# Optimization experiments

Measured on AMD Instinct MI355X. Metric: run time of the kernel, lower is better.

## Reference

```python
import jax, jax.numpy as jnp
import numpy as np

N = 1_000_000
C_IN = 64
COORD_SHIFT = 1024  # keeps shifted coords non-negative (offsets are small)


def setup_inputs() -> dict:
    key = jax.random.key(0)
    ks = jax.random.split(key, 8)
    feats = jax.random.normal(ks[0], (N, C_IN), dtype=jnp.float32)
    coords = jax.random.randint(ks[1], (N, 4), 0, 2048, dtype=jnp.int32)
    mask = jnp.ones((N,), dtype=bool)
    # Pointwise decoder params per decoder_blocks [(64,32),(32,16),(16,3)], bias=True
    s1, s2, s3 = 1.0 / np.sqrt(C_IN), 1.0 / np.sqrt(32), 1.0 / np.sqrt(16)
    W1 = jax.random.normal(ks[2], (C_IN, 32), dtype=jnp.float32) * s1
    b1 = jnp.zeros((32,), dtype=jnp.float32)
    W2 = jax.random.normal(ks[3], (32, 16), dtype=jnp.float32) * s2
    b2 = jnp.zeros((16,), dtype=jnp.float32)
    W3 = jax.random.normal(ks[4], (16, 3), dtype=jnp.float32) * s3
    b3 = jnp.zeros((3,), dtype=jnp.float32)
    return {"feats": feats, "coords": coords, "mask": mask,
            "W1": W1, "b1": b1, "W2": W2, "b2": b2, "W3": W3, "b3": b3}


def _decode(feats, mask, W1, b1, W2, b2, W3, b3):
    # FeatDecoder reduced to its pointwise (kernel-size-1 equivalent) form.
    h = jax.nn.relu(feats @ W1 + b1)
    h = jax.nn.relu(h @ W2 + b2)
    offsets = h @ W3 + b3  # [N, 3]
    return offsets * mask[:, None].astype(offsets.dtype)


def _revoxelize(offsets, coords):
    # offsets_ = [0 | round(offsets)] added to original coords
    off_i = jnp.round(offsets).astype(jnp.int32)                 # [N,3]
    new_coords = coords.at[:, 1:].add(off_i)                     # [N,4]
    # sphash -> unique -> sphashquery == row-wise unique with inverse map
    shifted = new_coords + COORD_SHIFT                           # non-negative rows
    _, inv = jnp.unique(shifted, axis=0, size=N, fill_value=0,
                        return_inverse=True)                      # inv: [N]
    inv = inv.reshape(-1).astype(jnp.int32)
    # spcount: voxels per cluster
    counts = jax.ops.segment_sum(jnp.ones((N,), jnp.float32), inv, num_segments=N)
    # spvoxelize: per-cluster mean of shifted coords, then .int()
    sums = jax.ops.segment_sum(new_coords.astype(jnp.float32), inv, num_segments=N)
    out_coords = (sums / jnp.maximum(counts, 1.0)[:, None]).astype(jnp.int32)
    return out_coords, inv


def reference(feats, coords, mask, W1, b1, W2, b2, W3, b3):
    offsets = _decode(feats, mask, W1, b1, W2, b2, W3, b3)
    out_coords, inv_map = _revoxelize(offsets, coords)
    return offsets, out_coords, inv_map
```

## Files before the change

### kernel.cpp

```cpp
#include <hip/hip_runtime.h>
#include <hip/hip_bf16.h>
#include <stdint.h>


#define TPB 256
#define NB 139264
#define NCHUNK 544
typedef unsigned long long ull;

__global__ __launch_bounds__(256) void k_mlp(
    const float* __restrict__ feats, const int* __restrict__ coords,
    const unsigned char* __restrict__ mask,
    const float* __restrict__ W1, const float* __restrict__ b1,
    const float* __restrict__ W2, const float* __restrict__ b2,
    const float* __restrict__ W3, const float* __restrict__ b3,
    float* __restrict__ out_off, ull* __restrict__ slots,
    unsigned int* __restrict__ cursor, int n)
{
    int i = blockIdx.x * TPB + threadIdx.x;
    if (i >= n) return;

    const float4* f4 = (const float4*)(feats + (size_t)i * 64);

    float h1[32];
    #pragma unroll
    for (int j = 0; j < 32; ++j) h1[j] = 0.0f;
    #pragma unroll
    for (int kc = 0; kc < 16; ++kc) {
        float4 xv = f4[kc];
        #pragma unroll
        for (int d = 0; d < 4; ++d) {
            float x = (d == 0) ? xv.x : (d == 1) ? xv.y : (d == 2) ? xv.z : xv.w;
            const float* wr = W1 + (kc * 4 + d) * 32;
            #pragma unroll
            for (int j = 0; j < 32; j += 4) {
                float4 w = *(const float4*)(wr + j);
                h1[j + 0] = fmaf(x, w.x, h1[j + 0]);
                h1[j + 1] = fmaf(x, w.y, h1[j + 1]);
                h1[j + 2] = fmaf(x, w.z, h1[j + 2]);
                h1[j + 3] = fmaf(x, w.w, h1[j + 3]);
            }
        }
    }
    #pragma unroll
    for (int j = 0; j < 32; ++j) h1[j] = fmaxf(h1[j] + b1[j], 0.0f);

    float h2[16];
    #pragma unroll
    for (int j = 0; j < 16; ++j) h2[j] = 0.0f;
    #pragma unroll
    for (int k = 0; k < 32; ++k) {
        float x = h1[k];
        const float* wr = W2 + k * 16;
        #pragma unroll
        for (int j = 0; j < 16; j += 4) {
            float4 w = *(const float4*)(wr + j);
            h2[j + 0] = fmaf(x, w.x, h2[j + 0]);
            h2[j + 1] = fmaf(x, w.y, h2[j + 1]);
            h2[j + 2] = fmaf(x, w.z, h2[j + 2]);
            h2[j + 3] = fmaf(x, w.w, h2[j + 3]);
        }
    }
    #pragma unroll
    for (int j = 0; j < 16; ++j) h2[j] = fmaxf(h2[j] + b2[j], 0.0f);

    float o0 = 0.0f, o1 = 0.0f, o2 = 0.0f;
    #pragma unroll
    for (int k = 0; k < 16; ++k) {
        float x = h2[k];
        o0 = fmaf(x, W3[k * 3 + 0], o0);
        o1 = fmaf(x, W3[k * 3 + 1], o1);
        o2 = fmaf(x, W3[k * 3 + 2], o2);
    }
    o0 += b3[0]; o1 += b3[1]; o2 += b3[2];

    float m = mask[i] ? 1.0f : 0.0f;
    o0 *= m; o1 *= m; o2 *= m;
    out_off[(size_t)3 * i + 0] = o0;
    out_off[(size_t)3 * i + 1] = o1;
    out_off[(size_t)3 * i + 2] = o2;

    int4 c = ((const int4*)coords)[i];
    int r1 = (int)rintf(o0), r2 = (int)rintf(o1), r3 = (int)rintf(o2);
    int c1u = c.y + r1, c2u = c.z + r2, c3u = c.w + r3;
    int c1s = min(max(c1u + 1024, 0), 8191);
    int c2s = min(max(c2u + 1024, 0), 8191);
    int c3s = min(max(c3u + 1024, 0), 8191);
    int bin1 = min(max((c1u + 64) >> 5, 0), 67);
    int b = c.x * 68 + bin1;
    ull row39 = ((ull)c1s << 26) | ((ull)c2s << 13) | (ull)c3s;
    ull packed = (row39 << 20) | (ull)(unsigned int)i;
    unsigned int j = atomicAdd(&cursor[b], 1u);
    if (j < 64u) slots[(size_t)b * 64 + j] = packed;
}

template<int W>
__device__ inline ull seg_sort(ull v, int lane)
{
    #pragma unroll
    for (int k = 2; k <= W; k <<= 1) {
        #pragma unroll
        for (int j = k >> 1; j > 0; j >>= 1) {
            ull o = __shfl_xor(v, j, 64);
            bool up = ((lane & (k & (W - 1))) == 0);
            bool lower = ((lane & j) == 0);
            ull mn = (v < o) ? v : o;
            ull mx = (v < o) ? o : v;
            v = (up == lower) ? mn : mx;
        }
    }
    return v;
}

__global__ __launch_bounds__(256) void k_passA(
    ull* __restrict__ slots, const unsigned int* __restrict__ cursor,
    unsigned int* __restrict__ ucnt, float* __restrict__ out_inv)
{
    int lane = threadIdx.x & 63;
    int b = blockIdx.x * 4 + (threadIdx.x >> 6);
    unsigned int cnt = cursor[b];
    if (cnt > 64u) cnt = 64u;
    if (cnt == 0u) { if (lane == 0) ucnt[b] = 0u; return; }
    ull v = (lane < (int)cnt) ? slots[(size_t)b * 64 + lane] : ~0ULL;
    if      (cnt <= 8u)  v = seg_sort<8>(v, lane);
    else if (cnt <= 16u) v = seg_sort<16>(v, lane);
    else if (cnt <= 32u) v = seg_sort<32>(v, lane);
    else                 v = seg_sort<64>(v, lane);

    ull row = v >> 20;
    unsigned int idx = (unsigned int)(v & 0xFFFFFULL);
    ull prev = __shfl_up(row, 1, 64);
    bool head = (lane < (int)cnt) && ((lane == 0) || (row != prev));
    ull hm = __ballot(head);
    ull le = (lane == 63) ? ~0ULL : ((1ULL << (lane + 1)) - 1ULL);
    int lrank = __popcll(hm & le) - 1;
    if (lane == 0) ucnt[b] = (unsigned int)__popcll(hm);
    if (lane < (int)cnt)
        ((unsigned int*)out_inv)[idx] = (unsigned int)(b * 64 + lrank);

    int c3s = (int)(row & 0x1FFFULL);
    int c2s = (int)((row >> 13) & 0x1FFFULL);
    int c1s = (int)(row >> 26);
    ull sum = (lane < (int)cnt)
        ? ((1ULL << 57) | ((ull)c1s << 38) | ((ull)c2s << 19) | (ull)c3s)
        : 0ULL;
    ull P = sum;
    #pragma unroll
    for (int d = 1; d < 64; d <<= 1) {
        ull t = __shfl_up(P, d, 64);
        if (lane >= d) P += t;
    }
    ull gt = hm & ~le;
    int tpos = gt ? (__ffsll((long long)gt) - 2) : ((int)cnt - 1);
    ull Pt = __shfl(P, tpos, 64);
    int hsrc = (lane > 0) ? lane - 1 : 0;
    ull Ph = __shfl(P, hsrc, 64);
    if (lane == 0) Ph = 0ULL;
    if (head) slots[(size_t)b * 64 + lrank] = Pt - Ph;
}

__global__ __launch_bounds__(256) void k_scanA(
    const unsigned int* __restrict__ ucnt, unsigned int* __restrict__ lstart,
    unsigned int* __restrict__ chsum)
{
    __shared__ unsigned int s[256];
    int tid = threadIdx.x;
    int g = blockIdx.x * 256 + tid;
    unsigned int v = ucnt[g];
    s[tid] = v;
    __syncthreads();
    for (int ofs = 1; ofs < 256; ofs <<= 1) {
        unsigned int t = (tid >= ofs) ? s[tid - ofs] : 0u;
        __syncthreads();
        s[tid] += t;
        __syncthreads();
    }
    lstart[g] = s[tid] - v;
    if (tid == 255) chsum[blockIdx.x] = s[255];
}

__global__ __launch_bounds__(1024) void k_scanB(unsigned int* __restrict__ chsum)
{
    __shared__ unsigned int s[1024];
    int tid = threadIdx.x;
    unsigned int v = (tid < NCHUNK) ? chsum[tid] : 0u;
    s[tid] = v;
    __syncthreads();
    for (int ofs = 1; ofs < 1024; ofs <<= 1) {
        unsigned int t = (tid >= ofs) ? s[tid - ofs] : 0u;
        __syncthreads();
        s[tid] += t;
        __syncthreads();
    }
    if (tid < NCHUNK) chsum[tid] = s[tid] - v;
}

__global__ __launch_bounds__(256) void k_fixinv(
    float* __restrict__ out_inv, const unsigned int* __restrict__ lstart,
    const unsigned int* __restrict__ chbase, int n)
{
    int i = blockIdx.x * TPB + threadIdx.x;
    if (i >= n) return;
    unsigned int q = ((const unsigned int*)out_inv)[i];
    unsigned int b = q >> 6, lr = q & 63u;
    if (b >= NB) b = NB - 1;
    out_inv[i] = (float)(chbase[b >> 8] + lstart[b] + lr);
}

__global__ __launch_bounds__(256) void k_fixout(
    const ull* __restrict__ slots, const unsigned int* __restrict__ ucnt,
    const unsigned int* __restrict__ lstart, const unsigned int* __restrict__ chbase,
    float* __restrict__ out_oc)
{
    int lane = threadIdx.x & 63;
    int b = blockIdx.x * 4 + (threadIdx.x >> 6);
    unsigned int uc = ucnt[b];
    if (lane >= (int)uc) return;
    ull run = slots[(size_t)b * 64 + lane];
    unsigned int r = chbase[b >> 8] + lstart[b] + (unsigned int)lane;
    int rc = (int)(run >> 57);
    int s1 = (int)((run >> 38) & 0x7FFFFULL) - 1024 * rc;
    int s2 = (int)((run >> 19) & 0x7FFFFULL) - 1024 * rc;
    int s3 = (int)(run & 0x7FFFFULL) - 1024 * rc;
    float fc = (float)rc;
    float4 o;
    o.x = (float)((unsigned int)b / 68u);
    o.y = truncf((float)s1 / fc);
    o.z = truncf((float)s2 / fc);
    o.w = truncf((float)s3 / fc);
    ((float4*)out_oc)[r] = o;
}

extern "C" void kernel_launch(void* const* d_in, const int* in_sizes, int n_in,
                              void* d_out, int out_size, void* d_ws, size_t ws_size,
                              hipStream_t stream)
{
    const float*         feats  = (const float*)d_in[0];
    const int*           coords = (const int*)d_in[1];
    const unsigned char* mask   = (const unsigned char*)d_in[2];
    const float* W1 = (const float*)d_in[3];
    const float* b1 = (const float*)d_in[4];
    const float* W2 = (const float*)d_in[5];
    const float* b2 = (const float*)d_in[6];
    const float* W3 = (const float*)d_in[7];
    const float* b3 = (const float*)d_in[8];

    int n = in_sizes[1] / 4;

    char* ws = (char*)d_ws;
    ull*          slots  = (ull*)ws;
    unsigned int* cursor = (unsigned int*)(ws + (size_t)NB * 64 * 8);
    unsigned int* ucnt   = cursor + NB;
    unsigned int* lstart = ucnt + NB;
    unsigned int* chsum  = lstart + NB;

    float* out     = (float*)d_out;
    float* out_off = out;
    float* out_oc  = out + (size_t)3 * n;
    float* out_inv = out + (size_t)7 * n;

    hipMemsetAsync(cursor, 0, (size_t)NB * sizeof(unsigned int), stream);
    hipMemsetAsync(out_oc, 0, (size_t)4 * n * sizeof(float), stream);

    int nb256 = (n + TPB - 1) / TPB;

    k_mlp<<<nb256, TPB, 0, stream>>>(feats, coords, mask, W1, b1, W2, b2, W3, b3,
                                     out_off, slots, cursor, n);
    k_passA<<<NB / 4, TPB, 0, stream>>>(slots, cursor, ucnt, out_inv);
    k_scanA<<<NCHUNK, 256, 0, stream>>>(ucnt, lstart, chsum);
    k_scanB<<<1, 1024, 0, stream>>>(chsum);
    k_fixinv<<<nb256, TPB, 0, stream>>>(out_inv, lstart, chsum, n);
    k_fixout<<<NB / 4, TPB, 0, stream>>>(slots, ucnt, lstart, chsum, out_oc);
}
```

Before: 543.0 us.

## Fuse inverse-fixup and output-coord kernels, prefetch features, specialize passA scan width

Merges k_fixinv and k_fixout into one per-point kernel, so each point computes its global cluster index and also writes that cluster's mean coordinates. This removes one launch and the separate bucket-parallel pass. Several points of the same cluster now redundantly write identical data, which adds extra slot reads and scattered stores. It also loads all 16 feature vectors up front behind an asm barrier to raise memory-level parallelism in the MLP, and templates passA so the prefix scan runs only over the active width.

```diff
diff --git a/kernel.cpp b/kernel.cpp
--- a/kernel.cpp
+++ b/kernel.cpp
@@ -7,6 +7,7 @@
 #define NB 139264
 #define NCHUNK 544
 typedef unsigned long long ull;
+typedef float vf4 __attribute__((ext_vector_type(4)));
 
 __global__ __launch_bounds__(256) void k_mlp(
     const float* __restrict__ feats, const int* __restrict__ coords,
@@ -20,14 +21,22 @@
     int i = blockIdx.x * TPB + threadIdx.x;
     if (i >= n) return;
 
-    const float4* f4 = (const float4*)(feats + (size_t)i * 64);
+    const vf4* f4 = (const vf4*)(feats + (size_t)i * 64);
+
+    vf4 r[16];
+    #pragma unroll
+    for (int p = 0; p < 16; ++p) r[p] = f4[p];
+    asm volatile("" : "+v"(r[0]), "+v"(r[1]), "+v"(r[2]), "+v"(r[3]),
+                      "+v"(r[4]), "+v"(r[5]), "+v"(r[6]), "+v"(r[7]),
+                      "+v"(r[8]), "+v"(r[9]), "+v"(r[10]), "+v"(r[11]),
+                      "+v"(r[12]), "+v"(r[13]), "+v"(r[14]), "+v"(r[15]));
 
     float h1[32];
     #pragma unroll
     for (int j = 0; j < 32; ++j) h1[j] = 0.0f;
     #pragma unroll
     for (int kc = 0; kc < 16; ++kc) {
-        float4 xv = f4[kc];
+        vf4 xv = r[kc];
         #pragma unroll
         for (int d = 0; d < 4; ++d) {
             float x = (d == 0) ? xv.x : (d == 1) ? xv.y : (d == 2) ? xv.z : xv.w;
@@ -112,20 +121,13 @@
     return v;
 }
 
-__global__ __launch_bounds__(256) void k_passA(
-    ull* __restrict__ slots, const unsigned int* __restrict__ cursor,
-    unsigned int* __restrict__ ucnt, float* __restrict__ out_inv)
-{
-    int lane = threadIdx.x & 63;
-    int b = blockIdx.x * 4 + (threadIdx.x >> 6);
-    unsigned int cnt = cursor[b];
-    if (cnt > 64u) cnt = 64u;
-    if (cnt == 0u) { if (lane == 0) ucnt[b] = 0u; return; }
+template<int W>
+__device__ inline void passA_body(
+    ull* __restrict__ slots, unsigned int* __restrict__ ucnt,
+    unsigned int* __restrict__ inv_bits, int b, int lane, unsigned int cnt)
+{
     ull v = (lane < (int)cnt) ? slots[(size_t)b * 64 + lane] : ~0ULL;
-    if      (cnt <= 8u)  v = seg_sort<8>(v, lane);
-    else if (cnt <= 16u) v = seg_sort<16>(v, lane);
-    else if (cnt <= 32u) v = seg_sort<32>(v, lane);
-    else                 v = seg_sort<64>(v, lane);
+    v = seg_sort<W>(v, lane);
 
     ull row = v >> 20;
     unsigned int idx = (unsigned int)(v & 0xFFFFFULL);
@@ -136,7 +138,7 @@
     int lrank = __popcll(hm & le) - 1;
     if (lane == 0) ucnt[b] = (unsigned int)__popcll(hm);
     if (lane < (int)cnt)
-        ((unsigned int*)out_inv)[idx] = (unsigned int)(b * 64 + lrank);
+        inv_bits[idx] = (unsigned int)(b * 64 + lrank);
 
     int c3s = (int)(row & 0x1FFFULL);
     int c2s = (int)((row >> 13) & 0x1FFFULL);
@@ -146,7 +148,7 @@
         : 0ULL;
     ull P = sum;
     #pragma unroll
-    for (int d = 1; d < 64; d <<= 1) {
+    for (int d = 1; d < W; d <<= 1) {
         ull t = __shfl_up(P, d, 64);
         if (lane >= d) P += t;
     }
@@ -157,6 +159,22 @@
     ull Ph = __shfl(P, hsrc, 64);
     if (lane == 0) Ph = 0ULL;
     if (head) slots[(size_t)b * 64 + lrank] = Pt - Ph;
+}
+
+__global__ __launch_bounds__(256) void k_passA(
+    ull* __restrict__ slots, const unsigned int* __restrict__ cursor,
+    unsigned int* __restrict__ ucnt, float* __restrict__ out_inv)
+{
+    int lane = threadIdx.x & 63;
+    int b = blockIdx.x * 4 + (threadIdx.x >> 6);
+    unsigned int cnt = cursor[b];
+    if (cnt > 64u) cnt = 64u;
+    if (cnt == 0u) { if (lane == 0) ucnt[b] = 0u; return; }
+    unsigned int* inv_bits = (unsigned int*)out_inv;
+    if      (cnt <= 8u)  passA_body<8> (slots, ucnt, inv_bits, b, lane, cnt);
+    else if (cnt <= 16u) passA_body<16>(slots, ucnt, inv_bits, b, lane, cnt);
+    else if (cnt <= 32u) passA_body<32>(slots, ucnt, inv_bits, b, lane, cnt);
+    else                 passA_body<64>(slots, ucnt, inv_bits, b, lane, cnt);
 }
 
 __global__ __launch_bounds__(256) void k_scanA(
@@ -195,8 +213,9 @@
     if (tid < NCHUNK) chsum[tid] = s[tid] - v;
 }
 
-__global__ __launch_bounds__(256) void k_fixinv(
-    float* __restrict__ out_inv, const unsigned int* __restrict__ lstart,
+__global__ __launch_bounds__(256) void k_final(
+    float* __restrict__ out_inv, float* __restrict__ out_oc,
+    const ull* __restrict__ slots, const unsigned int* __restrict__ lstart,
     const unsigned int* __restrict__ chbase, int n)
 {
     int i = blockIdx.x * TPB + threadIdx.x;
@@ -204,31 +223,22 @@
     unsigned int q = ((const unsigned int*)out_inv)[i];
     unsigned int b = q >> 6, lr = q & 63u;
     if (b >= NB) b = NB - 1;
-    out_inv[i] = (float)(chbase[b >> 8] + lstart[b] + lr);
-}
-
-__global__ __launch_bounds__(256) void k_fixout(
-    const ull* __restrict__ slots, const unsigned int* __restrict__ ucnt,
-    const unsigned int* __restrict__ lstart, const unsigned int* __restrict__ chbase,
-    float* __restrict__ out_oc)
-{
-    int lane = threadIdx.x & 63;
-    int b = blockIdx.x * 4 + (threadIdx.x >> 6);
-    unsigned int uc = ucnt[b];
-    if (lane >= (int)uc) return;
-    ull run = slots[(size_t)b * 64 + lane];
-    unsigned int r = chbase[b >> 8] + lstart[b] + (unsigned int)lane;
-    int rc = (int)(run >> 57);
-    int s1 = (int)((run >> 38) & 0x7FFFFULL) - 1024 * rc;
-    int s2 = (int)((run >> 19) & 0x7FFFFULL) - 1024 * rc;
-    int s3 = (int)(run & 0x7FFFFULL) - 1024 * rc;
-    float fc = (float)rc;
-    float4 o;
-    o.x = (float)((unsigned int)b / 68u);
-    o.y = truncf((float)s1 / fc);
-    o.z = truncf((float)s2 / fc);
-    o.w = truncf((float)s3 / fc);
-    ((float4*)out_oc)[r] = o;
+    unsigned int r = chbase[b >> 8] + lstart[b] + lr;
+    out_inv[i] = (float)r;
+    if (r < (unsigned int)n) {
+        ull run = slots[(size_t)b * 64 + lr];
+        int rc = (int)(run >> 57);
+        int s1 = (int)((run >> 38) & 0x7FFFFULL) - 1024 * rc;
+        int s2 = (int)((run >> 19) & 0x7FFFFULL) - 1024 * rc;
+        int s3 = (int)(run & 0x7FFFFULL) - 1024 * rc;
+        float fc = (float)rc;
+        float4 o;
+        o.x = (float)(b / 68u);
+        o.y = truncf((float)s1 / fc);
+        o.z = truncf((float)s2 / fc);
+        o.w = truncf((float)s3 / fc);
+        ((float4*)out_oc)[r] = o;
+    }
 }
 
 extern "C" void kernel_launch(void* const* d_in, const int* in_sizes, int n_in,
@@ -269,6 +279,5 @@
     k_passA<<<NB / 4, TPB, 0, stream>>>(slots, cursor, ucnt, out_inv);
     k_scanA<<<NCHUNK, 256, 0, stream>>>(ucnt, lstart, chsum);
     k_scanB<<<1, 1024, 0, stream>>>(chsum);
-    k_fixinv<<<nb256, TPB, 0, stream>>>(out_inv, lstart, chsum, n);
-    k_fixout<<<NB / 4, TPB, 0, stream>>>(slots, ucnt, lstart, chsum, out_oc);
-}
+    k_final<<<nb256, TPB, 0, stream>>>(out_inv, out_oc, slots, lstart, chsum, n);
+}
```

After: 530.5 us. 1.02x faster.
